# Kernel tuning notes

Measured on AMD Instinct MI355X. Metric: run time of the kernel, lower is better.

Reference implementation:

```python
import jax, jax.numpy as jnp
import numpy as np

T, N, E, F, H, OUT = 6, 50000, 800000, 32, 64, 16


def _glorot(key, shape):
    lim = np.sqrt(6.0 / (shape[0] + shape[1])).astype(np.float32)
    return jax.random.uniform(key, shape, jnp.float32, -lim, lim)


def setup_inputs() -> dict:
    key = jax.random.key(0)
    ks = jax.random.split(key, 12)
    return {
        "xs": jax.random.normal(ks[0], (T, N, F), jnp.float32),
        "edge_index": jax.random.randint(ks[1], (T, 2, E), 0, N, jnp.int32),
        # GCNConv weights/biases for the z, r, h gates
        "Wz": _glorot(ks[2], (F, H)), "bz": jnp.zeros((H,), jnp.float32),
        "Wr": _glorot(ks[3], (F, H)), "br": jnp.zeros((H,), jnp.float32),
        "Wh": _glorot(ks[4], (F, H)), "bh": jnp.zeros((H,), jnp.float32),
        # Linear(2H -> H) per gate
        "Lz_W": _glorot(ks[5], (2 * H, H)), "Lz_b": jnp.zeros((H,), jnp.float32),
        "Lr_W": _glorot(ks[6], (2 * H, H)), "Lr_b": jnp.zeros((H,), jnp.float32),
        "Lh_W": _glorot(ks[7], (2 * H, H)), "Lh_b": jnp.zeros((H,), jnp.float32),
        # final Linear(H -> 16)
        "out_W": _glorot(ks[8], (H, OUT)), "out_b": jnp.zeros((OUT,), jnp.float32),
    }


def _gcn(x, W, b, src, dst):
    """GCNConv: D^-1/2 (A+I) D^-1/2 X W + b, edge list form."""
    n = x.shape[0]
    xw = x @ W  # [N,H] project first (cheaper than per-edge)
    loop = jnp.arange(n, dtype=src.dtype)
    s = jnp.concatenate([src, loop])
    d = jnp.concatenate([dst, loop])
    deg = jax.ops.segment_sum(jnp.ones_like(d, jnp.float32), d, num_segments=n)
    dinv = jnp.where(deg > 0, jax.lax.rsqrt(deg), 0.0)
    norm = dinv[s] * dinv[d]          # [E+N]
    msg = xw[s] * norm[:, None]       # gather + scale
    agg = jax.ops.segment_sum(msg, d, num_segments=n)  # scatter-add
    return agg + b


def reference(xs, edge_index, Wz, bz, Wr, br, Wh, bh,
              Lz_W, Lz_b, Lr_W, Lr_b, Lh_W, Lh_b, out_W, out_b):
    n = xs.shape[1]

    def step(h, inp):
        x, src, dst = inp
        Z = jax.nn.sigmoid(jnp.concatenate([_gcn(x, Wz, bz, src, dst), h], -1) @ Lz_W + Lz_b)
        R = jax.nn.sigmoid(jnp.concatenate([_gcn(x, Wr, br, src, dst), h], -1) @ Lr_W + Lr_b)
        Ht = jnp.tanh(jnp.concatenate([_gcn(x, Wh, bh, src, dst), h * R], -1) @ Lh_W + Lh_b)
        h_new = Z * h + (1.0 - Z) * Ht
        return h_new, None

    h0 = jnp.zeros((n, Wz.shape[1]), xs.dtype)
    h_final, _ = jax.lax.scan(step, h0, (xs, edge_index[:, 0], edge_index[:, 1]))
    return h_final @ out_W + out_b  # [N,16]
```

## Files before the change

### kernel.cpp

```cpp
#include <hip/hip_runtime.h>
#include <hip/hip_bf16.h>

#define TT 6
#define NN 50000
#define EE 800000
#define FF 32
#define HH 64
#define OO 16

#define NB 256
#define DPB 196
#define CHUNK 4096
#define CAP 4096
#define SCAP 4608

#define WFRAG_N 19456

typedef unsigned short ushort_t;
typedef unsigned char uchar_t;
typedef short short8 __attribute__((ext_vector_type(8)));
typedef float f32x4 __attribute__((ext_vector_type(4)));
typedef float f32x2 __attribute__((ext_vector_type(2)));

__device__ __forceinline__ float ubf(ushort_t v){ return __uint_as_float(((unsigned)v) << 16); }
__device__ __forceinline__ ushort_t f2b(float f){
  unsigned u = __float_as_uint(f);
  return (ushort_t)((u + 0x7FFFu + ((u >> 16) & 1u)) >> 16);
}
__device__ __forceinline__ float lo16f(unsigned u){ return __uint_as_float(u << 16); }
__device__ __forceinline__ float hi16f(unsigned u){ return __uint_as_float(u & 0xFFFF0000u); }


__global__ void prepall_kernel(const float* __restrict__ Wz,const float* __restrict__ bz,
                               const float* __restrict__ Wr,const float* __restrict__ br,
                               const float* __restrict__ Wh,const float* __restrict__ bh,
                               const float* __restrict__ Lz,const float* __restrict__ Lzb,
                               const float* __restrict__ Lr,const float* __restrict__ Lrb,
                               const float* __restrict__ Lh,const float* __restrict__ Lhb,
                               const float* __restrict__ oW,const float* __restrict__ ob,
                               short* __restrict__ wfrag, float* __restrict__ wbias,
                               int* __restrict__ bcur){
  int bid = blockIdx.x, tid = threadIdx.x;
  if (bid < 76){
    int idx = bid*256 + tid;
    int slot = idx >> 9, lane = (idx >> 3) & 63, j = idx & 7;
    int q = lane >> 4, l15 = lane & 15;
    float val;
    if (slot < 36){
      int g, kc, ncol;
      if (slot < 24){ int nt = slot/3; kc = slot - nt*3; ncol = nt*16 + l15;
                      g = (ncol < 64) ? 0 : 1; ncol &= 63; }
      else          { int s2 = slot-24; int nt = s2/3; kc = s2 - nt*3;
                      ncol = nt*16 + l15; g = 2; }
      const float* W = (g==0)?Wz:((g==1)?Wr:Wh);
      const float* L = (g==0)?Lz:((g==1)?Lr:Lh);
      int k = kc*32 + q*8 + j;
      if (k < 32){
        float s = 0.f;
        for (int m = 0; m < 64; m++) s += W[k*64+m] * L[m*64+ncol];
        val = s;
      } else val = L[(32+k)*64 + ncol];
    } else {
      int kc = slot - 36;
      int k = kc*32 + q*8 + j;
      val = oW[k*16 + l15];
    }
    wfrag[idx] = (short)f2b(val);
  } else {
    if (tid < 192){
      int g = tid >> 6, j = tid & 63;
      const float* L  = (g==0)?Lz:((g==1)?Lr:Lh);
      const float* bb = (g==0)?bz:((g==1)?br:bh);
      const float* Lb = (g==0)?Lzb:((g==1)?Lrb:Lhb);
      float s = Lb[j];
      for (int m = 0; m < 64; m++) s += bb[m] * L[m*64+j];
      wbias[tid] = s;
    } else if (tid < 208){
      wbias[tid] = ob[tid-192];
    }
    for (int i = tid; i < 1536; i += 256) bcur[i] = 0;
  }
}

__global__ __launch_bounds__(256) void scatter_kernel(const int* __restrict__ ei,
                                                      int* __restrict__ bcur,
                                                      ushort_t* __restrict__ ssrc16,
                                                      uchar_t* __restrict__ sdst8){
  int t = blockIdx.y;
  __shared__ int cnt[NB];
  __shared__ int lstart[NB];
  __shared__ int gbase[NB];
  __shared__ int wsum[4];
  __shared__ ushort_t spay[CHUNK];
  __shared__ uchar_t  sdlo[CHUNK];
  __shared__ uchar_t  sbk[CHUNK];
  int tid = threadIdx.x;
  cnt[tid] = 0;
  __syncthreads();
  int e0 = blockIdx.x*CHUNK;
  const int* srcs = ei + t*2*EE;
  const int* dsts = ei + t*2*EE + EE;
  int pk[CHUNK/256];
  int ps[CHUNK/256];
  int pd[CHUNK/256];
  #pragma unroll
  for (int i = 0; i < CHUNK/256; i++){
    int e = e0 + i*256 + tid;
    if (e < EE){
      int s = srcs[e], d = dsts[e];
      int b = d / DPB;
      int lr = atomicAdd(&cnt[b], 1);
      pk[i] = (b << 12) | lr;
      ps[i] = s;
      pd[i] = d - b*DPB;
    } else pk[i] = -1;
  }
  __syncthreads();
  {
    int v = cnt[tid];
    int lane = tid & 63, wid = tid >> 6;
    int x = v;
    #pragma unroll
    for (int o = 1; o < 64; o <<= 1){
      int y = __shfl_up(x, o, 64);
      if (lane >= o) x += y;
    }
    if (lane == 63) wsum[wid] = x;
    __syncthreads();
    if (tid == 0){
      int s = 0;
      #pragma unroll
      for (int w = 0; w < 4; w++){ int tmp = wsum[w]; wsum[w] = s; s += tmp; }
    }
    __syncthreads();
    lstart[tid] = x - v + wsum[wid];
    gbase[tid] = (v > 0) ? atomicAdd(&bcur[t*NB + tid], v) : 0;
  }
  __syncthreads();
  #pragma unroll
  for (int i = 0; i < CHUNK/256; i++){
    if (pk[i] >= 0){
      int b = pk[i] >> 12, lr = pk[i] & 4095;
      int pos = lstart[b] + lr;
      spay[pos] = (ushort_t)ps[i];
      sdlo[pos] = (uchar_t)pd[i];
      sbk[pos]  = (uchar_t)b;
    }
  }
  __syncthreads();
  int nE = EE - e0; if (nE > CHUNK) nE = CHUNK;
  for (int i = tid; i < nE; i += 256){
    int b = sbk[i];
    int gpos = gbase[b] + (i - lstart[b]);
    if (gpos < CAP){
      size_t sb = (size_t)(t*NB + b)*CAP + gpos;
      ssrc16[sb] = spay[i];
      sdst8[sb]  = sdlo[i];
    }
  }
}

__global__ __launch_bounds__(256) void degdinv_kernel(const uchar_t* __restrict__ sdst8,
                                                      const int* __restrict__ bcur,
                                                      float* __restrict__ dinv,
                                                      int* __restrict__ ordg){
  int b = blockIdx.x, t = blockIdx.y, tid = threadIdx.x;
  __shared__ int cnt[DPB];
  __shared__ int wsum[4];
  __shared__ int dbase[64];
  for (int i = tid; i < DPB; i += 256) cnt[i] = 0;
  if (tid < 64) dbase[tid] = 0;
  __syncthreads();
  int ecnt = bcur[t*NB + b]; if (ecnt > CAP) ecnt = CAP;
  const uchar_t* dp = sdst8 + (size_t)(t*NB + b)*CAP;
  for (int i = tid; i < ecnt; i += 256)
    atomicAdd(&cnt[dp[i]], 1);
  __syncthreads();
  int v = (tid < DPB) ? cnt[tid] : 0;
  int pc = (v + 7) & ~7;
  int excl;
  {
    int lane = tid & 63, wid = tid >> 6;
    int x = pc;
    #pragma unroll
    for (int o = 1; o < 64; o <<= 1){
      int y = __shfl_up(x, o, 64);
      if (lane >= o) x += y;
    }
    if (lane == 63) wsum[wid] = x;
    __syncthreads();
    if (tid == 0){
      int s = 0;
      #pragma unroll
      for (int w = 0; w < 4; w++){ int tmp = wsum[w]; wsum[w] = s; s += tmp; }
    }
    __syncthreads();
    excl = x - pc + wsum[wid];
  }
  int cls = 63 - ((v > 63) ? 63 : v);
  if (tid < DPB) atomicAdd(&dbase[cls], 1);
  __syncthreads();
  if (tid == 0){
    int s = 0;
    for (int i = 0; i < 64; i++){ int c = dbase[i]; dbase[i] = s; s += c; }
  }
  __syncthreads();
  if (tid < DPB){
    int r = atomicAdd(&dbase[cls], 1);
    int cv = (v > 2047) ? 2047 : v;
    ordg[(size_t)(t*NB + b)*DPB + r] = (excl << 19) | (cv << 8) | tid;
  }
  for (int i = tid; i < DPB; i += 256){
    int n = b*DPB + i;
    if (n < NN) dinv[t*NN + n] = rsqrtf((float)(cnt[i] + 1));
  }
}

__global__ void cvtscale_kernel(const float4* __restrict__ x4,
                                const float* __restrict__ dinv,
                                ushort4* __restrict__ xb4){
  int i = blockIdx.x*256 + threadIdx.x;
  if (i < TT*NN*8){
    float dn = dinv[i >> 3];
    float4 v = x4[i];
    ushort4 o;
    o.x = f2b(v.x*dn); o.y = f2b(v.y*dn); o.z = f2b(v.z*dn); o.w = f2b(v.w*dn);
    xb4[i] = o;
  }
}

__global__ __launch_bounds__(256) void gatherb_kernel(const ushort_t* __restrict__ xbs,
                                                      const ushort_t* __restrict__ ssrc16,
                                                      const uchar_t* __restrict__ sdst8,
                                                      const int* __restrict__ bcur,
                                                      const int* __restrict__ ordg,
                                                      ushort_t* __restrict__ aggb){
  int l = blockIdx.x;
  int wk = ((l & 7) * 192) + (l >> 3);
  int t = wk >> 8;
  int b = wk & 255;
  int tid = threadIdx.x;
  __shared__ __align__(16) ushort_t ssrc[SCAP];
  __shared__ int sord[DPB];
  __shared__ int scnt[DPB];
  __shared__ int dcur;
  int ecnt = bcur[t*NB + b]; if (ecnt > CAP) ecnt = CAP;
  size_t slab = (size_t)(t*NB + b)*CAP;
  const ushort_t* sp = ssrc16 + slab;
  const uchar_t*  dp = sdst8 + slab;
  const int* og = ordg + (size_t)(t*NB + b)*DPB;
  if (tid < DPB){
    int e = og[tid];
    sord[tid] = e;
    scnt[e & 255] = (unsigned)e >> 19;
  }
  if (tid == 0) dcur = 0;
  __syncthreads();
  for (int e = tid; e < ecnt; e += 256){
    int d = dp[e];
    int pos = atomicAdd(&scnt[d], 1);
    if (pos < SCAP) ssrc[pos] = sp[e];
  }
  __syncthreads();
  int lane = tid & 63;
  int fp = lane & 7;
  const uint2* xb2 = (const uint2*)xbs + (size_t)t*NN*8;
  uint2* agg2 = (uint2*)aggb + (size_t)t*NN*8;
  while (true){
    int r = 0;
    if ((lane & 7) == 0) r = atomicAdd(&dcur, 1);
    r = __shfl(r, lane & 56, 64);
    if (r >= DPB) break;
    int pv = sord[r];
    int e0 = (unsigned)pv >> 19;
    int deg = (pv >> 8) & 2047;
    int ld = pv & 255;
    int e1 = e0 + deg;
    f32x2 a01 = {0.f, 0.f}, a23 = {0.f, 0.f};
    for (int i = e0; i < e1; i += 8){
      short8 sv = *(const short8*)&ssrc[i];
      uint2 rr[8];
      #pragma unroll
      for (int k = 0; k < 8; k++){
        int sidx = (int)(ushort_t)sv[k];
        rr[k] = xb2[(size_t)sidx*8 + fp];
      }
      int rem = e1 - i;
      #pragma unroll
      for (int k = 0; k < 8; k++){
        if (k >= rem){ rr[k].x = 0u; rr[k].y = 0u; }
        f32x2 v01 = {lo16f(rr[k].x), hi16f(rr[k].x)};
        f32x2 v23 = {lo16f(rr[k].y), hi16f(rr[k].y)};
        a01 += v01;
        a23 += v23;
      }
    }
    int n = b*DPB + ld;
    if (n < NN){
      float dn = rsqrtf((float)(deg + 1));
      uint2 sv = xb2[(size_t)n*8 + fp];
      float o0 = dn*(a01[0] + lo16f(sv.x));
      float o1 = dn*(a01[1] + hi16f(sv.x));
      float o2 = dn*(a23[0] + lo16f(sv.y));
      float o3 = dn*(a23[1] + hi16f(sv.y));
      uint2 pk;
      pk.x = (unsigned)f2b(o0) | ((unsigned)f2b(o1) << 16);
      pk.y = (unsigned)f2b(o2) | ((unsigned)f2b(o3) << 16);
      agg2[(size_t)n*8 + fp] = pk;
    }
  }
}

__global__ __launch_bounds__(256) void gates_kernel(const ushort_t* __restrict__ aggb,
                                                    const float* __restrict__ wbias,
                                                    const short* __restrict__ wfrag,
                                                    float* __restrict__ out){
  __shared__ __align__(16) short Hsp[4096];
  __shared__ __align__(16) short HRp[4096];
  int tid = threadIdx.x;
  int nb = blockIdx.x*64;
  int wv = tid >> 6, lane = tid & 63;
  int q = lane >> 4, l15 = lane & 15;
  #pragma unroll
  for (int r = 0; r < 8; r++) ((int*)Hsp)[tid + 256*r] = 0;
  short8 wz[3], wr[3], wh[3];
  #pragma unroll
  for (int kc = 0; kc < 3; kc++){
    wz[kc] = ((const short8*)wfrag)[(wv*3 + kc)*64 + lane];
    wr[kc] = ((const short8*)wfrag)[((wv+4)*3 + kc)*64 + lane];
    wh[kc] = ((const short8*)wfrag)[(24 + wv*3 + kc)*64 + lane];
  }
  int jz = wv*16 + l15;
  float cz = wbias[jz], cr = wbias[64 + jz], ch = wbias[128 + jz];
  int c0 = jz >> 3, jl = jz & 7, x0 = c0 & 7;
  int sq0 = q & 7, sq1 = (4 + q) & 7;
  float hreg[4][4];
  #pragma unroll
  for (int mt = 0; mt < 4; mt++)
    #pragma unroll
    for (int e = 0; e < 4; e++) hreg[mt][e] = 0.f;
  f32x4 accZ[4], accH[4];
  const short8* agf = (const short8*)aggb;
  for (int t = 0; t < TT; t++){
    short8 fac[4];
    #pragma unroll
    for (int mt = 0; mt < 4; mt++){
      int gn = nb + mt*16 + l15;
      short8 v = {0,0,0,0,0,0,0,0};
      if (gn < NN) v = agf[((size_t)t*NN + gn)*4 + q];
      fac[mt] = v;
    }
    __syncthreads();
    #pragma unroll
    for (int mt = 0; mt < 4; mt++){
      int n = mt*16 + l15;
      short8 fh0 = *(const short8*)&Hsp[((q)*64   + (n ^ sq0))*8];
      short8 fh1 = *(const short8*)&Hsp[((4+q)*64 + (n ^ sq1))*8];
      f32x4 az = {0.f,0.f,0.f,0.f}, ar = {0.f,0.f,0.f,0.f};
      az = __builtin_amdgcn_mfma_f32_16x16x32_bf16(fac[mt], wz[0], az, 0,0,0);
      az = __builtin_amdgcn_mfma_f32_16x16x32_bf16(fh0,     wz[1], az, 0,0,0);
      az = __builtin_amdgcn_mfma_f32_16x16x32_bf16(fh1,     wz[2], az, 0,0,0);
      ar = __builtin_amdgcn_mfma_f32_16x16x32_bf16(fac[mt], wr[0], ar, 0,0,0);
      ar = __builtin_amdgcn_mfma_f32_16x16x32_bf16(fh0,     wr[1], ar, 0,0,0);
      ar = __builtin_amdgcn_mfma_f32_16x16x32_bf16(fh1,     wr[2], ar, 0,0,0);
      accZ[mt] = az; accH[mt] = ar;
    }
    #pragma unroll
    for (int mt = 0; mt < 4; mt++){
      #pragma unroll
      for (int e = 0; e < 4; e++){
        int node = mt*16 + q*4 + e;
        float z = __builtin_amdgcn_rcpf(1.f + __expf(-(accZ[mt][e] + cz)));
        float r = __builtin_amdgcn_rcpf(1.f + __expf(-(accH[mt][e] + cr)));
        HRp[(c0*64 + (node ^ x0))*8 + jl] = (short)f2b(hreg[mt][e] * r);
        accZ[mt][e] = z;
      }
    }
    __syncthreads();
    #pragma unroll
    for (int mt = 0; mt < 4; mt++){
      int n = mt*16 + l15;
      short8 fr0 = *(const short8*)&HRp[((q)*64   + (n ^ sq0))*8];
      short8 fr1 = *(const short8*)&HRp[((4+q)*64 + (n ^ sq1))*8];
      f32x4 ahh = {0.f,0.f,0.f,0.f};
      ahh = __builtin_amdgcn_mfma_f32_16x16x32_bf16(fac[mt], wh[0], ahh, 0,0,0);
      ahh = __builtin_amdgcn_mfma_f32_16x16x32_bf16(fr0,     wh[1], ahh, 0,0,0);
      ahh = __builtin_amdgcn_mfma_f32_16x16x32_bf16(fr1,     wh[2], ahh, 0,0,0);
      accH[mt] = ahh;
    }
    #pragma unroll
    for (int mt = 0; mt < 4; mt++){
      #pragma unroll
      for (int e = 0; e < 4; e++){
        int node = mt*16 + q*4 + e;
        float xv = accH[mt][e] + ch;
        float ex = __expf(-2.f*fabsf(xv));
        float th = (1.f - ex) * __builtin_amdgcn_rcpf(1.f + ex);
        th = (xv < 0.f) ? -th : th;
        float z = accZ[mt][e];
        float hv = z*hreg[mt][e] + (1.f - z)*th;
        hreg[mt][e] = hv;
        Hsp[(c0*64 + (node ^ x0))*8 + jl] = (short)f2b(hv);
      }
    }
  }
  __syncthreads();
  short8 wo0 = ((const short8*)wfrag)[36*64 + lane];
  short8 wo1 = ((const short8*)wfrag)[37*64 + lane];
  int no = wv*16 + l15;
  short8 f0 = *(const short8*)&Hsp[((q)*64   + (no ^ sq0))*8];
  short8 f1 = *(const short8*)&Hsp[((4+q)*64 + (no ^ sq1))*8];
  f32x4 ao = {0.f,0.f,0.f,0.f};
  ao = __builtin_amdgcn_mfma_f32_16x16x32_bf16(f0, wo0, ao, 0,0,0);
  ao = __builtin_amdgcn_mfma_f32_16x16x32_bf16(f1, wo1, ao, 0,0,0);
  float ob = wbias[192 + l15];
  #pragma unroll
  for (int e = 0; e < 4; e++){
    int gn = nb + wv*16 + q*4 + e;
    if (gn < NN) out[gn*OO + l15] = ao[e] + ob;
  }
}

extern "C" void kernel_launch(void* const* d_in, const int* in_sizes, int n_in,
                              void* d_out, int out_size, void* d_ws, size_t ws_size,
                              hipStream_t stream) {
  const float* xs = (const float*)d_in[0];
  const int*   ei = (const int*)d_in[1];
  float* out = (float*)d_out;
  char* ws = (char*)d_ws;
  ushort_t*  aggb   = (ushort_t*)(ws + 0);
  ushort_t*  xbs    = (ushort_t*)(ws + 19200000);
  ushort_t*  ssrc16 = (ushort_t*)(ws + 38400000);
  uchar_t*   sdst8  = (uchar_t*) (ws + 50982912);
  float*     dinv   = (float*)   (ws + 57274368);
  int*       bcur   = (int*)     (ws + 58474368);
  short*     wfrag  = (short*)   (ws + 58480512);
  float*     wbias  = (float*)   (ws + 58519424);
  int*       ordg   = (int*)     (ws + 58520320);

  prepall_kernel<<<77, 256, 0, stream>>>(
      (const float*)d_in[2],(const float*)d_in[3],(const float*)d_in[4],(const float*)d_in[5],
      (const float*)d_in[6],(const float*)d_in[7],(const float*)d_in[8],(const float*)d_in[9],
      (const float*)d_in[10],(const float*)d_in[11],(const float*)d_in[12],(const float*)d_in[13],
      (const float*)d_in[14],(const float*)d_in[15], wfrag, wbias, bcur);
  scatter_kernel<<<dim3((EE + CHUNK-1)/CHUNK, TT), 256, 0, stream>>>(ei, bcur, ssrc16, sdst8);
  degdinv_kernel<<<dim3(NB, TT), 256, 0, stream>>>(sdst8, bcur, dinv, ordg);
  cvtscale_kernel<<<(TT*NN*8 + 255)/256, 256, 0, stream>>>((const float4*)xs, dinv, (ushort4*)xbs);
  gatherb_kernel<<<NB*TT, 256, 0, stream>>>(xbs, ssrc16, sdst8, bcur, ordg, aggb);
  gates_kernel<<<(NN + 63)/64, 256, 0, stream>>>(aggb, wbias, wfrag, out);
}
```

Measured before the change: 240.0 us.

## Compute degrees with global atomics in scatter and fold ordering into gather

Removes the separate degree/dinv kernel. Node degrees are now counted with global atomicAdd in the scatter pass into a zeroed array, cvtscale computes rsqrt on the fly, and the degree-sorted ordering and prefix scan move into the gather kernel's prologue. This saves one launch and the re-read of sdst8, but adds 4.8M global atomics spread over random addresses plus a zeroing pass in the prep kernel.

```diff
diff --git a/kernel.cpp b/kernel.cpp
--- a/kernel.cpp
+++ b/kernel.cpp
@@ -10,6 +10,7 @@
 
 #define NB 256
 #define DPB 196
+#define DEGN 50176
 #define CHUNK 4096
 #define CAP 4096
 #define SCAP 4608
@@ -39,7 +40,7 @@
                                const float* __restrict__ Lh,const float* __restrict__ Lhb,
                                const float* __restrict__ oW,const float* __restrict__ ob,
                                short* __restrict__ wfrag, float* __restrict__ wbias,
-                               int* __restrict__ bcur){
+                               int* __restrict__ bcur, int* __restrict__ deg){
   int bid = blockIdx.x, tid = threadIdx.x;
   if (bid < 76){
     int idx = bid*256 + tid;
@@ -66,7 +67,7 @@
       val = oW[k*16 + l15];
     }
     wfrag[idx] = (short)f2b(val);
-  } else {
+  } else if (bid == 76){
     if (tid < 192){
       int g = tid >> 6, j = tid & 63;
       const float* L  = (g==0)?Lz:((g==1)?Lr:Lh);
@@ -79,13 +80,17 @@
       wbias[tid] = ob[tid-192];
     }
     for (int i = tid; i < 1536; i += 256) bcur[i] = 0;
+  } else {
+    int i = (bid - 77)*1024 + tid*4;
+    if (i < TT*DEGN) *(int4*)&deg[i] = make_int4(0,0,0,0);
   }
 }
 
 __global__ __launch_bounds__(256) void scatter_kernel(const int* __restrict__ ei,
                                                       int* __restrict__ bcur,
                                                       ushort_t* __restrict__ ssrc16,
-                                                      uchar_t* __restrict__ sdst8){
+                                                      uchar_t* __restrict__ sdst8,
+                                                      int* __restrict__ deg){
   int t = blockIdx.y;
   __shared__ int cnt[NB];
   __shared__ int lstart[NB];
@@ -100,6 +105,7 @@
   int e0 = blockIdx.x*CHUNK;
   const int* srcs = ei + t*2*EE;
   const int* dsts = ei + t*2*EE + EE;
+  int* degt = deg + (size_t)t*DEGN;
   int pk[CHUNK/256];
   int ps[CHUNK/256];
   int pd[CHUNK/256];
@@ -110,6 +116,7 @@
       int s = srcs[e], d = dsts[e];
       int b = d / DPB;
       int lr = atomicAdd(&cnt[b], 1);
+      atomicAdd(&degt[d], 1);
       pk[i] = (b << 12) | lr;
       ps[i] = s;
       pd[i] = d - b*DPB;
@@ -160,72 +167,18 @@
   }
 }
 
-__global__ __launch_bounds__(256) void degdinv_kernel(const uchar_t* __restrict__ sdst8,
-                                                      const int* __restrict__ bcur,
-                                                      float* __restrict__ dinv,
-                                                      int* __restrict__ ordg){
-  int b = blockIdx.x, t = blockIdx.y, tid = threadIdx.x;
-  __shared__ int cnt[DPB];
-  __shared__ int wsum[4];
-  __shared__ int dbase[64];
-  for (int i = tid; i < DPB; i += 256) cnt[i] = 0;
-  if (tid < 64) dbase[tid] = 0;
-  __syncthreads();
-  int ecnt = bcur[t*NB + b]; if (ecnt > CAP) ecnt = CAP;
-  const uchar_t* dp = sdst8 + (size_t)(t*NB + b)*CAP;
-  for (int i = tid; i < ecnt; i += 256)
-    atomicAdd(&cnt[dp[i]], 1);
-  __syncthreads();
-  int v = (tid < DPB) ? cnt[tid] : 0;
-  int pc = (v + 7) & ~7;
-  int excl;
-  {
-    int lane = tid & 63, wid = tid >> 6;
-    int x = pc;
-    #pragma unroll
-    for (int o = 1; o < 64; o <<= 1){
-      int y = __shfl_up(x, o, 64);
-      if (lane >= o) x += y;
-    }
-    if (lane == 63) wsum[wid] = x;
-    __syncthreads();
-    if (tid == 0){
-      int s = 0;
-      #pragma unroll
-      for (int w = 0; w < 4; w++){ int tmp = wsum[w]; wsum[w] = s; s += tmp; }
-    }
-    __syncthreads();
-    excl = x - pc + wsum[wid];
-  }
-  int cls = 63 - ((v > 63) ? 63 : v);
-  if (tid < DPB) atomicAdd(&dbase[cls], 1);
-  __syncthreads();
-  if (tid == 0){
-    int s = 0;
-    for (int i = 0; i < 64; i++){ int c = dbase[i]; dbase[i] = s; s += c; }
-  }
-  __syncthreads();
-  if (tid < DPB){
-    int r = atomicAdd(&dbase[cls], 1);
-    int cv = (v > 2047) ? 2047 : v;
-    ordg[(size_t)(t*NB + b)*DPB + r] = (excl << 19) | (cv << 8) | tid;
-  }
-  for (int i = tid; i < DPB; i += 256){
-    int n = b*DPB + i;
-    if (n < NN) dinv[t*NN + n] = rsqrtf((float)(cnt[i] + 1));
-  }
-}
-
 __global__ void cvtscale_kernel(const float4* __restrict__ x4,
-                                const float* __restrict__ dinv,
+                                const int* __restrict__ deg,
                                 ushort4* __restrict__ xb4){
-  int i = blockIdx.x*256 + threadIdx.x;
-  if (i < TT*NN*8){
-    float dn = dinv[i >> 3];
-    float4 v = x4[i];
+  int t = blockIdx.y;
+  int idx = blockIdx.x*256 + threadIdx.x;
+  if (idx < NN*8){
+    int n = idx >> 3;
+    float dn = rsqrtf((float)(deg[(size_t)t*DEGN + n] + 1));
+    float4 v = x4[(size_t)t*NN*8 + idx];
     ushort4 o;
     o.x = f2b(v.x*dn); o.y = f2b(v.y*dn); o.z = f2b(v.z*dn); o.w = f2b(v.w*dn);
-    xb4[i] = o;
+    xb4[(size_t)t*NN*8 + idx] = o;
   }
 }
 
@@ -233,7 +186,7 @@
                                                       const ushort_t* __restrict__ ssrc16,
                                                       const uchar_t* __restrict__ sdst8,
                                                       const int* __restrict__ bcur,
-                                                      const int* __restrict__ ordg,
+                                                      const int* __restrict__ deg,
                                                       ushort_t* __restrict__ aggb){
   int l = blockIdx.x;
   int wk = ((l & 7) * 192) + (l >> 3);
@@ -243,26 +196,58 @@
   __shared__ __align__(16) ushort_t ssrc[SCAP];
   __shared__ int sord[DPB];
   __shared__ int scnt[DPB];
+  __shared__ int wsum[4];
+  __shared__ int dbase[64];
   __shared__ int dcur;
+  if (tid < 64) dbase[tid] = 0;
+  if (tid == 0) dcur = 0;
+  int v = (tid < DPB) ? deg[(size_t)t*DEGN + b*DPB + tid] : 0;
+  int pc = (v + 7) & ~7;
+  int lane = tid & 63, wid = tid >> 6;
+  {
+    int x = pc;
+    #pragma unroll
+    for (int o = 1; o < 64; o <<= 1){
+      int y = __shfl_up(x, o, 64);
+      if (lane >= o) x += y;
+    }
+    if (lane == 63) wsum[wid] = x;
+    __syncthreads();
+    if (tid == 0){
+      int s = 0;
+      #pragma unroll
+      for (int w = 0; w < 4; w++){ int tmp = wsum[w]; wsum[w] = s; s += tmp; }
+    }
+    __syncthreads();
+    int excl = x - pc + wsum[wid];
+    int cls = 63 - ((v > 63) ? 63 : v);
+    if (tid < DPB){
+      scnt[tid] = excl;
+      atomicAdd(&dbase[cls], 1);
+    }
+    __syncthreads();
+    if (tid == 0){
+      int s = 0;
+      for (int i = 0; i < 64; i++){ int c = dbase[i]; dbase[i] = s; s += c; }
+    }
+    __syncthreads();
+    if (tid < DPB){
+      int r = atomicAdd(&dbase[cls], 1);
+      int cv = (v > 2047) ? 2047 : v;
+      sord[r] = (excl << 19) | (cv << 8) | tid;
+    }
+  }
+  __syncthreads();
   int ecnt = bcur[t*NB + b]; if (ecnt > CAP) ecnt = CAP;
   size_t slab = (size_t)(t*NB + b)*CAP;
   const ushort_t* sp = ssrc16 + slab;
   const uchar_t*  dp = sdst8 + slab;
-  const int* og = ordg + (size_t)(t*NB + b)*DPB;
-  if (tid < DPB){
-    int e = og[tid];
-    sord[tid] = e;
-    scnt[e & 255] = (unsigned)e >> 19;
-  }
-  if (tid == 0) dcur = 0;
-  __syncthreads();
   for (int e = tid; e < ecnt; e += 256){
     int d = dp[e];
     int pos = atomicAdd(&scnt[d], 1);
     if (pos < SCAP) ssrc[pos] = sp[e];
   }
   __syncthreads();
-  int lane = tid & 63;
   int fp = lane & 7;
   const uint2* xb2 = (const uint2*)xbs + (size_t)t*NN*8;
   uint2* agg2 = (uint2*)aggb + (size_t)t*NN*8;
@@ -273,9 +258,9 @@
     if (r >= DPB) break;
     int pv = sord[r];
     int e0 = (unsigned)pv >> 19;
-    int deg = (pv >> 8) & 2047;
+    int dg = (pv >> 8) & 2047;
     int ld = pv & 255;
-    int e1 = e0 + deg;
+    int e1 = e0 + dg;
     f32x2 a01 = {0.f, 0.f}, a23 = {0.f, 0.f};
     for (int i = e0; i < e1; i += 8){
       short8 sv = *(const short8*)&ssrc[i];
@@ -297,7 +282,7 @@
     }
     int n = b*DPB + ld;
     if (n < NN){
-      float dn = rsqrtf((float)(deg + 1));
+      float dn = rsqrtf((float)(dg + 1));
       uint2 sv = xb2[(size_t)n*8 + fp];
       float o0 = dn*(a01[0] + lo16f(sv.x));
       float o1 = dn*(a01[1] + hi16f(sv.x));
@@ -432,20 +417,18 @@
   ushort_t*  xbs    = (ushort_t*)(ws + 19200000);
   ushort_t*  ssrc16 = (ushort_t*)(ws + 38400000);
   uchar_t*   sdst8  = (uchar_t*) (ws + 50982912);
-  float*     dinv   = (float*)   (ws + 57274368);
   int*       bcur   = (int*)     (ws + 58474368);
   short*     wfrag  = (short*)   (ws + 58480512);
   float*     wbias  = (float*)   (ws + 58519424);
-  int*       ordg   = (int*)     (ws + 58520320);
-
-  prepall_kernel<<<77, 256, 0, stream>>>(
+  int*       deg    = (int*)     (ws + 58520320);
+
+  prepall_kernel<<<371, 256, 0, stream>>>(
       (const float*)d_in[2],(const float*)d_in[3],(const float*)d_in[4],(const float*)d_in[5],
       (const float*)d_in[6],(const float*)d_in[7],(const float*)d_in[8],(const float*)d_in[9],
       (const float*)d_in[10],(const float*)d_in[11],(const float*)d_in[12],(const float*)d_in[13],
-      (const float*)d_in[14],(const float*)d_in[15], wfrag, wbias, bcur);
-  scatter_kernel<<<dim3((EE + CHUNK-1)/CHUNK, TT), 256, 0, stream>>>(ei, bcur, ssrc16, sdst8);
-  degdinv_kernel<<<dim3(NB, TT), 256, 0, stream>>>(sdst8, bcur, dinv, ordg);
-  cvtscale_kernel<<<(TT*NN*8 + 255)/256, 256, 0, stream>>>((const float4*)xs, dinv, (ushort4*)xbs);
-  gatherb_kernel<<<NB*TT, 256, 0, stream>>>(xbs, ssrc16, sdst8, bcur, ordg, aggb);
+      (const float*)d_in[14],(const float*)d_in[15], wfrag, wbias, bcur, deg);
+  scatter_kernel<<<dim3((EE + CHUNK-1)/CHUNK, TT), 256, 0, stream>>>(ei, bcur, ssrc16, sdst8, deg);
+  cvtscale_kernel<<<dim3((NN*8 + 255)/256, TT), 256, 0, stream>>>((const float4*)xs, deg, (ushort4*)xbs);
+  gatherb_kernel<<<NB*TT, 256, 0, stream>>>(xbs, ssrc16, sdst8, bcur, deg, aggb);
   gates_kernel<<<(NN + 63)/64, 256, 0, stream>>>(aggb, wbias, wfrag, out);
 }
```

Result: slower. 406.4 us (+69.4%).
